# Performance work log

Hardware: AMD Instinct MI355X
Metric: run time of the kernel (lower is better)

## Reference

```python
import jax, jax.numpy as jnp
import numpy as np

B = 2048
NUM_CLASSES = 16384
FEAT_DIM = 2048


def setup_inputs() -> dict:
    key = jax.random.key(0)
    kx, kc, kl = jax.random.split(key, 3)
    x = jax.random.normal(kx, (B, FEAT_DIM), dtype=jnp.float32)
    centers = jax.random.normal(kc, (NUM_CLASSES, FEAT_DIM), dtype=jnp.float32)
    labels = jax.random.randint(kl, (B,), 0, NUM_CLASSES, dtype=jnp.int64)
    return {"x": x, "labels": labels, "centers": centers}


def reference(x, labels, centers):
    # Faithful to the torch module: full [B, C] squared-distance matrix,
    # then select the true-label entry per row (boolean-mask picks one per row).
    x_sq = jnp.sum(x * x, axis=1, keepdims=True)              # [B, 1]
    c_sq = jnp.sum(centers * centers, axis=1)[None, :]        # [1, C]
    distmat = x_sq + c_sq - 2.0 * (x @ centers.T)             # [B, C]
    dist = jnp.take_along_axis(distmat, labels[:, None], axis=1)[:, 0]  # [B]
    loss = jnp.mean(jnp.clip(dist, 1e-12, 1e12))
    return loss
```

## Files before the change

kernel.cpp:

```cpp
#include <hip/hip_runtime.h>


#define FEAT_DIM 2048
#define BATCH 2048

__global__ __launch_bounds__(256) void center_dist_kernel(
    const float* __restrict__ x,
    const int* __restrict__ labels,
    const float* __restrict__ centers,
    float* __restrict__ dist_ws) {
    const int row  = blockIdx.x * 4 + (threadIdx.x >> 6);
    const int lane = threadIdx.x & 63;
    const int lbl  = labels[row];
    const float4* xr = reinterpret_cast<const float4*>(x + (size_t)row * FEAT_DIM);
    const float4* cr = reinterpret_cast<const float4*>(centers + (size_t)lbl * FEAT_DIM);

    float sx2 = 0.f, sc2 = 0.f, sxc = 0.f;
    #pragma unroll
    for (int j = 0; j < (FEAT_DIM / 4) / 64; ++j) {
        float4 xv = xr[lane + 64 * j];
        float4 cv = cr[lane + 64 * j];
        sx2 += xv.x * xv.x + xv.y * xv.y + xv.z * xv.z + xv.w * xv.w;
        sc2 += cv.x * cv.x + cv.y * cv.y + cv.z * cv.z + cv.w * cv.w;
        sxc += xv.x * cv.x + xv.y * cv.y + xv.z * cv.z + xv.w * cv.w;
    }

    #pragma unroll
    for (int off = 32; off > 0; off >>= 1) {
        sx2 += __shfl_down(sx2, off, 64);
        sc2 += __shfl_down(sc2, off, 64);
        sxc += __shfl_down(sxc, off, 64);
    }

    if (lane == 0) {
        float d = sx2 + sc2 - 2.0f * sxc;
        d = fminf(fmaxf(d, 1e-12f), 1e12f);
        dist_ws[row] = d;
    }
}

__global__ __launch_bounds__(64) void mean_kernel(
    const float* __restrict__ dist_ws, float* __restrict__ out) {
    const float4* dw = reinterpret_cast<const float4*>(dist_ws);
    float s = 0.f;
    #pragma unroll
    for (int j = 0; j < (BATCH / 4) / 64; ++j) {
        float4 v = dw[threadIdx.x + 64 * j];
        s += v.x + v.y + v.z + v.w;
    }
    #pragma unroll
    for (int off = 32; off > 0; off >>= 1) s += __shfl_down(s, off, 64);
    if (threadIdx.x == 0) out[0] = s / (float)BATCH;
}

extern "C" void kernel_launch(void* const* d_in, const int* in_sizes, int n_in,
                              void* d_out, int out_size, void* d_ws, size_t ws_size,
                              hipStream_t stream) {
    const float* x = (const float*)d_in[0];
    const int* labels = (const int*)d_in[1];
    const float* centers = (const float*)d_in[2];
    float* out = (float*)d_out;
    float* dist_ws = (float*)d_ws;

    center_dist_kernel<<<BATCH / 4, 256, 0, stream>>>(x, labels, centers, dist_ws);
    mean_kernel<<<1, 64, 0, stream>>>(dist_ws, out);
}
```

Measured before the change: 11.47 us.

## Fuse mean reduction into distance kernel via spin-waited packed workspace

Replaces the two-kernel distance-then-mean pipeline with one kernel. Each wave writes its clamped distance as a 64-bit word holding the value and its bitwise complement. Block 0 spin-waits on those words until every entry validates, then reduces them to the mean, removing the second launch and its gap. The distance is also computed directly as the sum of (x-c)^2 instead of the expanded x²+c²-2xc form, which cuts arithmetic. The risk is that stale valid words left in the workspace from a previous call pass the check, so block 0 can read old values, and the spin-wait depends on other blocks getting scheduled.

```diff
diff --git a/kernel.cpp b/kernel.cpp
--- a/kernel.cpp
+++ b/kernel.cpp
@@ -1,56 +1,67 @@
 #include <hip/hip_runtime.h>
+#include <stdint.h>
 
 
 #define FEAT_DIM 2048
 #define BATCH 2048
+#define THREADS 256
+#define NBLK (BATCH / 4)
 
-__global__ __launch_bounds__(256) void center_dist_kernel(
+__global__ __launch_bounds__(THREADS) void center_loss_kernel(
     const float* __restrict__ x,
     const int* __restrict__ labels,
     const float* __restrict__ centers,
-    float* __restrict__ dist_ws) {
-    const int row  = blockIdx.x * 4 + (threadIdx.x >> 6);
+    float* __restrict__ out,
+    uint64_t* __restrict__ pair_ws) {
+    const int wave = threadIdx.x >> 6;
     const int lane = threadIdx.x & 63;
+    const int row  = blockIdx.x * 4 + wave;
     const int lbl  = labels[row];
     const float4* xr = reinterpret_cast<const float4*>(x + (size_t)row * FEAT_DIM);
     const float4* cr = reinterpret_cast<const float4*>(centers + (size_t)lbl * FEAT_DIM);
 
-    float sx2 = 0.f, sc2 = 0.f, sxc = 0.f;
+    float s = 0.f;
     #pragma unroll
     for (int j = 0; j < (FEAT_DIM / 4) / 64; ++j) {
         float4 xv = xr[lane + 64 * j];
         float4 cv = cr[lane + 64 * j];
-        sx2 += xv.x * xv.x + xv.y * xv.y + xv.z * xv.z + xv.w * xv.w;
-        sc2 += cv.x * cv.x + cv.y * cv.y + cv.z * cv.z + cv.w * cv.w;
-        sxc += xv.x * cv.x + xv.y * cv.y + xv.z * cv.z + xv.w * cv.w;
+        float dx = xv.x - cv.x, dy = xv.y - cv.y;
+        float dz = xv.z - cv.z, dw = xv.w - cv.w;
+        s += dx * dx + dy * dy + dz * dz + dw * dw;
     }
 
     #pragma unroll
-    for (int off = 32; off > 0; off >>= 1) {
-        sx2 += __shfl_down(sx2, off, 64);
-        sc2 += __shfl_down(sc2, off, 64);
-        sxc += __shfl_down(sxc, off, 64);
+    for (int off = 32; off > 0; off >>= 1) s += __shfl_down(s, off, 64);
+
+    if (lane == 0) {
+        float d = fminf(fmaxf(s, 1e-12f), 1e12f);
+        uint32_t lo = __float_as_uint(d);
+        uint64_t pk = ((uint64_t)(~lo) << 32) | (uint64_t)lo;
+        __hip_atomic_store(&pair_ws[row], pk, __ATOMIC_RELEASE,
+                           __HIP_MEMORY_SCOPE_AGENT);
     }
 
-    if (lane == 0) {
-        float d = sx2 + sc2 - 2.0f * sxc;
-        d = fminf(fmaxf(d, 1e-12f), 1e12f);
-        dist_ws[row] = d;
+    if (blockIdx.x == 0) {
+        float part = 0.f;
+        #pragma unroll
+        for (int j = 0; j < BATCH / THREADS; ++j) {
+            const int i = threadIdx.x + j * THREADS;
+            uint64_t v;
+            do {
+                v = __hip_atomic_load(&pair_ws[i], __ATOMIC_ACQUIRE,
+                                      __HIP_MEMORY_SCOPE_AGENT);
+            } while ((uint32_t)(v >> 32) != ~(uint32_t)v);
+            part += __uint_as_float((uint32_t)v);
+        }
+        #pragma unroll
+        for (int off = 32; off > 0; off >>= 1) part += __shfl_down(part, off, 64);
+
+        __shared__ float red[4];
+        if (lane == 0) red[wave] = part;
+        __syncthreads();
+        if (threadIdx.x == 0)
+            out[0] = (red[0] + red[1] + red[2] + red[3]) / (float)BATCH;
     }
-}
-
-__global__ __launch_bounds__(64) void mean_kernel(
-    const float* __restrict__ dist_ws, float* __restrict__ out) {
-    const float4* dw = reinterpret_cast<const float4*>(dist_ws);
-    float s = 0.f;
-    #pragma unroll
-    for (int j = 0; j < (BATCH / 4) / 64; ++j) {
-        float4 v = dw[threadIdx.x + 64 * j];
-        s += v.x + v.y + v.z + v.w;
-    }
-    #pragma unroll
-    for (int off = 32; off > 0; off >>= 1) s += __shfl_down(s, off, 64);
-    if (threadIdx.x == 0) out[0] = s / (float)BATCH;
 }
 
 extern "C" void kernel_launch(void* const* d_in, const int* in_sizes, int n_in,
@@ -60,8 +71,8 @@
     const int* labels = (const int*)d_in[1];
     const float* centers = (const float*)d_in[2];
     float* out = (float*)d_out;
-    float* dist_ws = (float*)d_ws;
+    uint64_t* pair_ws = (uint64_t*)d_ws;
 
-    center_dist_kernel<<<BATCH / 4, 256, 0, stream>>>(x, labels, centers, dist_ws);
-    mean_kernel<<<1, 64, 0, stream>>>(dist_ws, out);
+    center_loss_kernel<<<NBLK, THREADS, 0, stream>>>(x, labels, centers, out,
+                                                     pair_ws);
 }
```

New measurement: 30.80 us. 168% more time.

## Compute direct squared difference and pre-reduce per block before mean

Applied to the files above, without the earlier changes.

Replaces the three-accumulator expansion (x², c², x·c) with a direct sum of squared differences, cutting arithmetic and shuffle reductions to one accumulator. Each block now handles 8 rows with 512 threads and reduces its clamped distances in shared memory into one partial, so the mean kernel reads 256 partials with a single float4 per lane. The kernel is memory-bound on gathering rows, so compute savings are small; the larger block adds a __syncthreads.

```diff
diff --git a/kernel.cpp b/kernel.cpp
--- a/kernel.cpp
+++ b/kernel.cpp
@@ -3,51 +3,51 @@
 
 #define FEAT_DIM 2048
 #define BATCH 2048
+#define ROWS_PER_BLK 8
+#define NBLK (BATCH / ROWS_PER_BLK)
 
-__global__ __launch_bounds__(256) void center_dist_kernel(
+__global__ __launch_bounds__(512) void center_dist_kernel(
     const float* __restrict__ x,
     const int* __restrict__ labels,
     const float* __restrict__ centers,
-    float* __restrict__ dist_ws) {
-    const int row  = blockIdx.x * 4 + (threadIdx.x >> 6);
+    float* __restrict__ partial_ws) {
+    const int wave = threadIdx.x >> 6;
     const int lane = threadIdx.x & 63;
+    const int row  = blockIdx.x * ROWS_PER_BLK + wave;
     const int lbl  = labels[row];
     const float4* xr = reinterpret_cast<const float4*>(x + (size_t)row * FEAT_DIM);
     const float4* cr = reinterpret_cast<const float4*>(centers + (size_t)lbl * FEAT_DIM);
 
-    float sx2 = 0.f, sc2 = 0.f, sxc = 0.f;
+    float s = 0.f;
     #pragma unroll
     for (int j = 0; j < (FEAT_DIM / 4) / 64; ++j) {
         float4 xv = xr[lane + 64 * j];
         float4 cv = cr[lane + 64 * j];
-        sx2 += xv.x * xv.x + xv.y * xv.y + xv.z * xv.z + xv.w * xv.w;
-        sc2 += cv.x * cv.x + cv.y * cv.y + cv.z * cv.z + cv.w * cv.w;
-        sxc += xv.x * cv.x + xv.y * cv.y + xv.z * cv.z + xv.w * cv.w;
+        float dx = xv.x - cv.x, dy = xv.y - cv.y;
+        float dz = xv.z - cv.z, dw = xv.w - cv.w;
+        s += dx * dx + dy * dy + dz * dz + dw * dw;
     }
 
     #pragma unroll
-    for (int off = 32; off > 0; off >>= 1) {
-        sx2 += __shfl_down(sx2, off, 64);
-        sc2 += __shfl_down(sc2, off, 64);
-        sxc += __shfl_down(sxc, off, 64);
-    }
+    for (int off = 32; off > 0; off >>= 1) s += __shfl_down(s, off, 64);
 
-    if (lane == 0) {
-        float d = sx2 + sc2 - 2.0f * sxc;
-        d = fminf(fmaxf(d, 1e-12f), 1e12f);
-        dist_ws[row] = d;
+    __shared__ float red[ROWS_PER_BLK];
+    if (lane == 0)
+        red[wave] = fminf(fmaxf(s, 1e-12f), 1e12f);
+    __syncthreads();
+    if (threadIdx.x == 0) {
+        float p = 0.f;
+        #pragma unroll
+        for (int w = 0; w < ROWS_PER_BLK; ++w) p += red[w];
+        partial_ws[blockIdx.x] = p;
     }
 }
 
 __global__ __launch_bounds__(64) void mean_kernel(
-    const float* __restrict__ dist_ws, float* __restrict__ out) {
-    const float4* dw = reinterpret_cast<const float4*>(dist_ws);
-    float s = 0.f;
-    #pragma unroll
-    for (int j = 0; j < (BATCH / 4) / 64; ++j) {
-        float4 v = dw[threadIdx.x + 64 * j];
-        s += v.x + v.y + v.z + v.w;
-    }
+    const float* __restrict__ partial_ws, float* __restrict__ out) {
+    const float4* pw = reinterpret_cast<const float4*>(partial_ws);
+    float4 v = pw[threadIdx.x];
+    float s = (v.x + v.y) + (v.z + v.w);
     #pragma unroll
     for (int off = 32; off > 0; off >>= 1) s += __shfl_down(s, off, 64);
     if (threadIdx.x == 0) out[0] = s / (float)BATCH;
@@ -60,8 +60,8 @@
     const int* labels = (const int*)d_in[1];
     const float* centers = (const float*)d_in[2];
     float* out = (float*)d_out;
-    float* dist_ws = (float*)d_ws;
+    float* partial_ws = (float*)d_ws;
 
-    center_dist_kernel<<<BATCH / 4, 256, 0, stream>>>(x, labels, centers, dist_ws);
-    mean_kernel<<<1, 64, 0, stream>>>(dist_ws, out);
+    center_dist_kernel<<<NBLK, 512, 0, stream>>>(x, labels, centers, partial_ws);
+    mean_kernel<<<1, 64, 0, stream>>>(partial_ws, out);
 }
```

Result: slower. 11.74 us (+2.4%).
